# Optimization experiments

Hardware: AMD Instinct MI355X
Metric: run time of the kernel (lower is better)

## Reference

```python
import jax, jax.numpy as jnp
import numpy as np

C = 256          # channel dim, forced by self.cal (256x256)
POOL_K = 16      # feature_hw // proto_grid = 256 // 16
THRESH = 0.5
A_COEF = 0.2     # self.a


def build_cal():
    # tridiagonal 'cal' parameter from get_wight()
    cal = np.eye(C, dtype=np.float32)
    for i in range(C - 2):
        cal[i + 1, i] = 0.3
        cal[i + 1, i + 1] = 0.8
        cal[i + 1, i + 2] = 0.3
    return jnp.asarray(cal)


def setup_inputs() -> dict:
    key = jax.random.key(0)
    k1, k2, k3, k4 = jax.random.split(key, 4)
    qry = jax.random.normal(k1, (1, 1, C, 256, 256), jnp.float32)      # [way, nb, C, H, W]
    sup_x = jax.random.normal(k2, (1, 1, 1, C, 256, 256), jnp.float32)  # [way, shot, nb, C, H, W]
    sup_y = jax.random.uniform(k3, (1, 1, 1, 256, 256), jnp.float32)    # [way, shot, nb, H, W]
    s_init_seed = jax.random.randint(k4, (1, 100, 2), 0, 256)           # unused in 'gridconv'
    return {"qry": qry, "sup_x": sup_x, "sup_y": sup_y,
            "s_init_seed": s_init_seed, "cal": build_cal()}


def avg_pool(x, k):
    b, c, h, w = x.shape
    return x.reshape(b, c, h // k, k, w // k, k).mean(axis=(3, 5))


def safe_norm(x, axis, eps=1e-4):
    n = jnp.maximum(jnp.linalg.norm(x, axis=axis, keepdims=True), eps)
    return x / n


def reference(qry, sup_x, sup_y, s_init_seed, cal):
    # squeezes from the original forward
    qry = qry[:, 0]          # [1, C, H, W]
    sup_x = sup_x[0, :, 0]   # [shot, C, H, W]
    sup_y = sup_y[0]         # [shot, 1, H, W]
    ns, c, H, W = sup_x.shape

    # avg-pool support features into grid prototypes -> X: [C, N]
    nsx = avg_pool(sup_x, POOL_K)                                  # [ns, C, Gh, Gw]
    X = nsx.reshape(ns, c, -1).transpose(0, 2, 1).reshape(-1, c).T  # [C, N]

    # channel-affinity refinement: A = 1 + a * band_mask * softmax(X X^T); w3 = A * cal
    w1 = X @ X.T                                                   # [C, C]
    soft = jax.nn.softmax(w1, axis=1)
    idx = jnp.arange(c)
    mask_w = (jnp.abs(idx[:, None] - idx[None, :]) <= 1).astype(X.dtype)  # wts_near band
    A = 1.0 + A_COEF * mask_w * soft
    Xn = (A * cal) @ X                                             # [C, N]

    # pooled support mask -> proto selection
    sup_y_g = avg_pool(sup_y, POOL_K).reshape(ns, 1, -1).transpose(1, 0, 2).reshape(-1)  # [N]
    sel = sup_y_g > THRESH

    protos = safe_norm(Xn.T, axis=1)   # [N, C]
    qry_n = safe_norm(qry, axis=1)     # [1, C, H, W]

    # 1x1 conv cosine similarity; mask unselected protos (equiv. to boolean filtering)
    dists = jnp.einsum('bchw,nc->bnhw', qry_n, protos) * 20.0
    dists = jnp.where(sel[None, :, None, None], dists, jnp.float32(-1e9))
    attn = jax.nn.softmax(dists, axis=1)
    pred_grid = jnp.sum(attn * dists, axis=1, keepdims=True)       # [1, 1, H, W]
    debug_assign = jnp.argmax(dists, axis=1).astype(jnp.float32)
    return (pred_grid, debug_assign)
```

## Files before the change

### kernel.cpp

```cpp
#include <hip/hip_runtime.h>
#include <math.h>

#define CC 256
#define HW 65536
#define SS 256

#define WS_XT    0
#define WS_BORD  0
#define WS_XN    98304
#define WS_YG    163840
#define WS_INVN  164096
#define WS_SELF  164352

typedef __attribute__((ext_vector_type(8))) short short8;
typedef __attribute__((ext_vector_type(4))) float f32x4;

__device__ inline unsigned short bf16_rne(float f) {
    unsigned int u = __float_as_uint(f);
    return (unsigned short)((u + 0x7fffu + ((u >> 16) & 1u)) >> 16);
}
__device__ inline float bf16_f(unsigned short h) {
    return __uint_as_float(((unsigned int)h) << 16);
}

__global__ void pool_kernel(const float* __restrict__ sup_x,
                            const float* __restrict__ sup_y,
                            float* __restrict__ ws) {
    int blk = blockIdx.x;
    int t   = threadIdx.x;
    const float* src = (blk < CC) ? (sup_x + (size_t)blk * HW) : sup_y;

    for (int py = 0; py < 16; ++py) {
        float acc = 0.f;
        int hbase = py * 16;
        #pragma unroll
        for (int i = 0; i < 16; ++i)
            acc += src[(hbase + i) * 256 + t];
        acc += __shfl_down(acc, 8, 16);
        acc += __shfl_down(acc, 4, 16);
        acc += __shfl_down(acc, 2, 16);
        acc += __shfl_down(acc, 1, 16);
        if ((t & 15) == 0) {
            int cell = py * 16 + (t >> 4);
            float v = acc * (1.f / 256.f);
            if (blk < CC) ws[WS_XT + cell * SS + blk] = v;
            else          ws[WS_YG + cell] = v;
        }
    }
}

__global__ void calib_kernel(const float* __restrict__ cal,
                             float* __restrict__ ws) {
    int i = blockIdx.x;
    int j = threadIdx.x;
    const float* Xt = ws + WS_XT;
    float* Xn = ws + WS_XN;

    __shared__ float xi[SS];
    __shared__ float red[256];
    __shared__ float e[CC];
    __shared__ float T[3];

    xi[j] = Xt[j * SS + i];
    __syncthreads();

    float d0 = 0.f, d1 = 0.f, d2 = 0.f, d3 = 0.f;
    #pragma unroll 4
    for (int s = 0; s < SS; s += 4) {
        d0 += xi[s + 0] * Xt[(s + 0) * SS + j];
        d1 += xi[s + 1] * Xt[(s + 1) * SS + j];
        d2 += xi[s + 2] * Xt[(s + 2) * SS + j];
        d3 += xi[s + 3] * Xt[(s + 3) * SS + j];
    }
    float dot = (d0 + d1) + (d2 + d3);

    red[j] = dot; __syncthreads();
    for (int off = 128; off > 0; off >>= 1) {
        if (j < off) red[j] = fmaxf(red[j], red[j + off]);
        __syncthreads();
    }
    float m = red[0];
    __syncthreads();

    float ev = expf(dot - m);
    e[j] = ev;
    red[j] = ev; __syncthreads();
    for (int off = 128; off > 0; off >>= 1) {
        if (j < off) red[j] += red[j + off];
        __syncthreads();
    }
    float esum = red[0];
    __syncthreads();

    if (j < 3) {
        int jj = i + j - 1;
        float tv = 0.f;
        if (jj >= 0 && jj < CC) {
            float soft = e[jj] / esum;
            tv = (1.f + 0.2f * soft) * cal[i * CC + jj];
        }
        T[j] = tv;
    }
    __syncthreads();

    float v = T[1] * xi[j];
    if (i > 0)      v += T[0] * Xt[j * SS + i - 1];
    if (i < CC - 1) v += T[2] * Xt[j * SS + i + 1];
    Xn[i * SS + j] = v;
}

__global__ void prep_kernel(float* __restrict__ ws) {
    int b = blockIdx.x;
    int t = threadIdx.x;
    int nn = t & 31, cg = t >> 5;
    int n = b * 32 + nn;
    const float* Xn = ws + WS_XN;
    float s = 0.f;
    #pragma unroll 8
    for (int c = cg * 32; c < cg * 32 + 32; ++c) {
        float v = Xn[c * SS + n];
        s += v * v;
    }
    __shared__ float red[256];
    red[t] = s;
    __syncthreads();
    if (t < 32) {
        float acc = 0.f;
        #pragma unroll
        for (int g = 0; g < 8; ++g) acc += red[g * 32 + t];
        ws[WS_INVN + n] = 1.f / fmaxf(sqrtf(acc), 1e-4f);
        ws[WS_SELF + n] = (ws[WS_YG + n] > 0.5f) ? 1.f : 0.f;
    }
}

__global__ void bprep_kernel(float* __restrict__ ws) {
    int rem = (blockIdx.x & 3) * 256 + threadIdx.x;
    int c = blockIdx.x >> 2;
    int t = rem >> 6, L = rem & 63;
    int quad = L >> 4, nh = L & 15;
    int n = t * 16 + nh;
    int kb = c * 32 + quad * 8;
    const float* Xn = ws + WS_XN;

    union { unsigned short u[8]; uint4 v; } hh, mm, ll;
    #pragma unroll
    for (int j = 0; j < 8; ++j) {
        float f = Xn[(kb + j) * SS + n];
        unsigned short h = bf16_rne(f);
        float f1 = f - bf16_f(h);
        unsigned short m = bf16_rne(f1);
        float f2 = f1 - bf16_f(m);
        unsigned short l = bf16_rne(f2);
        hh.u[j] = h; mm.u[j] = m; ll.u[j] = l;
    }
    unsigned short* bord = (unsigned short*)(ws + WS_BORD);
    size_t base = ((((size_t)c * 3) * 16 + t) * 64 + L) * 8;
    *reinterpret_cast<uint4*>(&bord[base])         = hh.v;
    *reinterpret_cast<uint4*>(&bord[base + 8192])  = mm.v;
    *reinterpret_cast<uint4*>(&bord[base + 16384]) = ll.v;
}

#define NCH 8

__global__ __launch_bounds__(256)
void main_kernel(const float* __restrict__ qry,
                 const float* __restrict__ ws,
                 float* __restrict__ out) {
    __shared__ float pm[64 * 65];
    __shared__ float pa[64 * 65];
    __shared__ float invqs[64];
    __shared__ float mfin[64];
    __shared__ float afin[64];

    int tid = threadIdx.x;
    int lane = tid & 63, w = tid >> 6;
    int quad = lane >> 4, nh = lane & 15;
    int p0 = blockIdx.x * 64;
    const unsigned short* bord = (const unsigned short*)(ws + WS_BORD);

    f32x4 acc[4][4];
    #pragma unroll
    for (int mt = 0; mt < 4; ++mt)
        #pragma unroll
        for (int nt = 0; nt < 4; ++nt)
            acc[mt][nt] = (f32x4){0.f, 0.f, 0.f, 0.f};

    float qsq[4] = {0.f, 0.f, 0.f, 0.f};

    #pragma unroll 1
    for (int c = 0; c < NCH; ++c) {
        int k0 = c * 32 + quad * 8;
        short8 afr[4][3];
        #pragma unroll
        for (int mt = 0; mt < 4; ++mt) {
            float v[8];
            #pragma unroll
            for (int j = 0; j < 8; ++j)
                v[j] = qry[(size_t)(k0 + j) * HW + p0 + mt * 16 + nh];
            short8 ah, am, al;
            #pragma unroll
            for (int j = 0; j < 8; ++j) {
                qsq[mt] += v[j] * v[j];
                unsigned short h = bf16_rne(v[j]);
                float f1 = v[j] - bf16_f(h);
                unsigned short m = bf16_rne(f1);
                float f2 = f1 - bf16_f(m);
                unsigned short l = bf16_rne(f2);
                ah[j] = (short)h; am[j] = (short)m; al[j] = (short)l;
            }
            afr[mt][0] = ah; afr[mt][1] = am; afr[mt][2] = al;
        }

        const unsigned short* bc = bord + (size_t)c * 24576;
        #pragma unroll
        for (int nt = 0; nt < 4; ++nt) {
            int tg = w * 4 + nt;
            short8 bh = *(const short8*)&bc[(size_t)((0 * 16 + tg) * 64 + lane) * 8];
            short8 bm = *(const short8*)&bc[(size_t)((1 * 16 + tg) * 64 + lane) * 8];
            short8 bl = *(const short8*)&bc[(size_t)((2 * 16 + tg) * 64 + lane) * 8];
            #pragma unroll
            for (int mt = 0; mt < 4; ++mt) {
                f32x4 a = acc[mt][nt];
                a = __builtin_amdgcn_mfma_f32_16x16x32_bf16(afr[mt][2], bh, a, 0, 0, 0);
                a = __builtin_amdgcn_mfma_f32_16x16x32_bf16(afr[mt][0], bl, a, 0, 0, 0);
                a = __builtin_amdgcn_mfma_f32_16x16x32_bf16(afr[mt][1], bm, a, 0, 0, 0);
                a = __builtin_amdgcn_mfma_f32_16x16x32_bf16(afr[mt][1], bh, a, 0, 0, 0);
                a = __builtin_amdgcn_mfma_f32_16x16x32_bf16(afr[mt][0], bm, a, 0, 0, 0);
                a = __builtin_amdgcn_mfma_f32_16x16x32_bf16(afr[mt][0], bh, a, 0, 0, 0);
                acc[mt][nt] = a;
            }
        }
    }

    #pragma unroll
    for (int mt = 0; mt < 4; ++mt) {
        qsq[mt] += __shfl_xor(qsq[mt], 16);
        qsq[mt] += __shfl_xor(qsq[mt], 32);
    }
    if (w == 0 && quad == 0) {
        #pragma unroll
        for (int mt = 0; mt < 4; ++mt)
            invqs[mt * 16 + nh] = 1.f / fmaxf(sqrtf(qsq[mt]), 1e-4f);
    }

    float invn4[4], self4[4];
    #pragma unroll
    for (int nt = 0; nt < 4; ++nt) {
        int n = w * 64 + nt * 16 + nh;
        invn4[nt] = ws[WS_INVN + n];
        self4[nt] = ws[WS_SELF + n];
    }
    __syncthreads();

    #pragma unroll
    for (int mt = 0; mt < 4; ++mt) {
        #pragma unroll
        for (int r = 0; r < 4; ++r) {
            int p = mt * 16 + quad * 4 + r;
            float iq = invqs[p] * 20.f;
            float bv = -3.4e38f, ba = 1e9f;
            #pragma unroll
            for (int nt = 0; nt < 4; ++nt) {
                float d = acc[mt][nt][r] * invn4[nt] * iq;
                d = (self4[nt] > 0.5f) ? d : -1e9f;
                acc[mt][nt][r] = d;
                float na = (float)(w * 64 + nt * 16 + nh);
                if (d > bv || (d == bv && na < ba)) { bv = d; ba = na; }
            }
            pm[p * 65 + w * 16 + nh] = bv;
            pa[p * 65 + w * 16 + nh] = ba;
        }
    }
    __syncthreads();

    {
        int p = tid >> 2, q4 = tid & 3;
        float bv = -3.4e38f, ba = 1e9f;
        #pragma unroll
        for (int jj = 0; jj < 16; ++jj) {
            int cx = q4 * 16 + jj;
            float v2 = pm[p * 65 + cx];
            float a2 = pa[p * 65 + cx];
            if (v2 > bv || (v2 == bv && a2 < ba)) { bv = v2; ba = a2; }
        }
        #pragma unroll
        for (int off = 1; off < 4; off <<= 1) {
            float ov = __shfl_xor(bv, off, 4);
            float oa = __shfl_xor(ba, off, 4);
            if (ov > bv || (ov == bv && oa < ba)) { bv = ov; ba = oa; }
        }
        if (q4 == 0) { mfin[p] = bv; afin[p] = ba; }
    }
    __syncthreads();

    #pragma unroll
    for (int mt = 0; mt < 4; ++mt) {
        #pragma unroll
        for (int r = 0; r < 4; ++r) {
            int p = mt * 16 + quad * 4 + r;
            float m = mfin[p];
            float s1 = 0.f, s2 = 0.f;
            #pragma unroll
            for (int nt = 0; nt < 4; ++nt) {
                float d = acc[mt][nt][r];
                float ev = expf(d - m);
                s1 += ev;
                s2 += ev * d;
            }
            pm[p * 65 + w * 16 + nh] = s1;
            pa[p * 65 + w * 16 + nh] = s2;
        }
    }
    __syncthreads();

    {
        int p = tid >> 2, q4 = tid & 3;
        float s1 = 0.f, s2 = 0.f;
        #pragma unroll
        for (int jj = 0; jj < 16; ++jj) {
            int cx = q4 * 16 + jj;
            s1 += pm[p * 65 + cx];
            s2 += pa[p * 65 + cx];
        }
        #pragma unroll
        for (int off = 1; off < 4; off <<= 1) {
            s1 += __shfl_xor(s1, off, 4);
            s2 += __shfl_xor(s2, off, 4);
        }
        if (q4 == 0) {
            out[p0 + p]      = s2 / s1;
            out[HW + p0 + p] = afin[p];
        }
    }
}

extern "C" void kernel_launch(void* const* d_in, const int* in_sizes, int n_in,
                              void* d_out, int out_size, void* d_ws, size_t ws_size,
                              hipStream_t stream) {
    const float* qry   = (const float*)d_in[0];
    const float* sup_x = (const float*)d_in[1];
    const float* sup_y = (const float*)d_in[2];
    const float* cal   = (const float*)d_in[4];
    float* out = (float*)d_out;
    float* ws  = (float*)d_ws;

    pool_kernel<<<257, 256, 0, stream>>>(sup_x, sup_y, ws);
    calib_kernel<<<256, 256, 0, stream>>>(cal, ws);
    prep_kernel<<<8, 256, 0, stream>>>(ws);
    bprep_kernel<<<32, 256, 0, stream>>>(ws);
    main_kernel<<<HW / 64, 256, 0, stream>>>(qry, ws, out);
}
```

Measured before the change: 232.4 us.

## Prefetch query chunks, truncate bf16 splits, merge prep kernels, split pooling blocks

In the main kernel, the next channel chunk of query values is loaded into registers while the current chunk is converted and fed to MFMA, which hides global-load latency. The three-way bf16 split of the query now truncates instead of rounding to nearest, which costs fewer ALU ops per element. The prep and bprep kernels are merged into one launch, and pooling uses twice as many blocks, each covering half the rows. These changes add register pressure in the main kernel and slightly change the precision of the split.

```diff
diff --git a/kernel.cpp b/kernel.cpp
--- a/kernel.cpp
+++ b/kernel.cpp
@@ -28,9 +28,12 @@
                             float* __restrict__ ws) {
     int blk = blockIdx.x;
     int t   = threadIdx.x;
-    const float* src = (blk < CC) ? (sup_x + (size_t)blk * HW) : sup_y;
-
-    for (int py = 0; py < 16; ++py) {
+    int ch   = (blk < 512) ? (blk >> 1) : CC;
+    int pyb  = (blk < 512) ? ((blk & 1) * 8) : 0;
+    int pye  = (blk < 512) ? (pyb + 8) : 16;
+    const float* src = (blk < 512) ? (sup_x + (size_t)ch * HW) : sup_y;
+
+    for (int py = pyb; py < pye; ++py) {
         float acc = 0.f;
         int hbase = py * 16;
         #pragma unroll
@@ -43,8 +46,8 @@
         if ((t & 15) == 0) {
             int cell = py * 16 + (t >> 4);
             float v = acc * (1.f / 256.f);
-            if (blk < CC) ws[WS_XT + cell * SS + blk] = v;
-            else          ws[WS_YG + cell] = v;
+            if (blk < 512) ws[WS_XT + cell * SS + ch] = v;
+            else           ws[WS_YG + cell] = v;
         }
     }
 }
@@ -109,55 +112,55 @@
     Xn[i * SS + j] = v;
 }
 
-__global__ void prep_kernel(float* __restrict__ ws) {
-    int b = blockIdx.x;
-    int t = threadIdx.x;
-    int nn = t & 31, cg = t >> 5;
-    int n = b * 32 + nn;
+__global__ void prep_bprep_kernel(float* __restrict__ ws) {
     const float* Xn = ws + WS_XN;
-    float s = 0.f;
-    #pragma unroll 8
-    for (int c = cg * 32; c < cg * 32 + 32; ++c) {
-        float v = Xn[c * SS + n];
-        s += v * v;
-    }
-    __shared__ float red[256];
-    red[t] = s;
-    __syncthreads();
-    if (t < 32) {
-        float acc = 0.f;
-        #pragma unroll
-        for (int g = 0; g < 8; ++g) acc += red[g * 32 + t];
-        ws[WS_INVN + n] = 1.f / fmaxf(sqrtf(acc), 1e-4f);
-        ws[WS_SELF + n] = (ws[WS_YG + n] > 0.5f) ? 1.f : 0.f;
-    }
-}
-
-__global__ void bprep_kernel(float* __restrict__ ws) {
-    int rem = (blockIdx.x & 3) * 256 + threadIdx.x;
-    int c = blockIdx.x >> 2;
-    int t = rem >> 6, L = rem & 63;
-    int quad = L >> 4, nh = L & 15;
-    int n = t * 16 + nh;
-    int kb = c * 32 + quad * 8;
-    const float* Xn = ws + WS_XN;
-
-    union { unsigned short u[8]; uint4 v; } hh, mm, ll;
-    #pragma unroll
-    for (int j = 0; j < 8; ++j) {
-        float f = Xn[(kb + j) * SS + n];
-        unsigned short h = bf16_rne(f);
-        float f1 = f - bf16_f(h);
-        unsigned short m = bf16_rne(f1);
-        float f2 = f1 - bf16_f(m);
-        unsigned short l = bf16_rne(f2);
-        hh.u[j] = h; mm.u[j] = m; ll.u[j] = l;
-    }
-    unsigned short* bord = (unsigned short*)(ws + WS_BORD);
-    size_t base = ((((size_t)c * 3) * 16 + t) * 64 + L) * 8;
-    *reinterpret_cast<uint4*>(&bord[base])         = hh.v;
-    *reinterpret_cast<uint4*>(&bord[base + 8192])  = mm.v;
-    *reinterpret_cast<uint4*>(&bord[base + 16384]) = ll.v;
+    if (blockIdx.x < 8) {
+        int b = blockIdx.x;
+        int t = threadIdx.x;
+        int nn = t & 31, cg = t >> 5;
+        int n = b * 32 + nn;
+        float s = 0.f;
+        #pragma unroll 8
+        for (int c = cg * 32; c < cg * 32 + 32; ++c) {
+            float v = Xn[c * SS + n];
+            s += v * v;
+        }
+        __shared__ float red[256];
+        red[t] = s;
+        __syncthreads();
+        if (t < 32) {
+            float acc = 0.f;
+            #pragma unroll
+            for (int g = 0; g < 8; ++g) acc += red[g * 32 + t];
+            ws[WS_INVN + n] = 1.f / fmaxf(sqrtf(acc), 1e-4f);
+            ws[WS_SELF + n] = (ws[WS_YG + n] > 0.5f) ? 1.f : 0.f;
+        }
+    } else {
+        int blk = blockIdx.x - 8;
+        int rem = (blk & 3) * 256 + threadIdx.x;
+        int c = blk >> 2;
+        int t = rem >> 6, L = rem & 63;
+        int quad = L >> 4, nh = L & 15;
+        int n = t * 16 + nh;
+        int kb = c * 32 + quad * 8;
+
+        union { unsigned short u[8]; uint4 v; } hh, mm, ll;
+        #pragma unroll
+        for (int j = 0; j < 8; ++j) {
+            float f = Xn[(kb + j) * SS + n];
+            unsigned short h = bf16_rne(f);
+            float f1 = f - bf16_f(h);
+            unsigned short m = bf16_rne(f1);
+            float f2 = f1 - bf16_f(m);
+            unsigned short l = bf16_rne(f2);
+            hh.u[j] = h; mm.u[j] = m; ll.u[j] = l;
+        }
+        unsigned short* bord = (unsigned short*)(ws + WS_BORD);
+        size_t base = ((((size_t)c * 3) * 16 + t) * 64 + L) * 8;
+        *reinterpret_cast<uint4*>(&bord[base])         = hh.v;
+        *reinterpret_cast<uint4*>(&bord[base + 8192])  = mm.v;
+        *reinterpret_cast<uint4*>(&bord[base + 16384]) = ll.v;
+    }
 }
 
 #define NCH 8
@@ -177,6 +180,7 @@
     int quad = lane >> 4, nh = lane & 15;
     int p0 = blockIdx.x * 64;
     const unsigned short* bord = (const unsigned short*)(ws + WS_BORD);
+    const float* qb = qry + p0 + nh;
 
     f32x4 acc[4][4];
     #pragma unroll
@@ -187,28 +191,41 @@
 
     float qsq[4] = {0.f, 0.f, 0.f, 0.f};
 
+    float va[4][8];
+    #pragma unroll
+    for (int mt = 0; mt < 4; ++mt)
+        #pragma unroll
+        for (int j = 0; j < 8; ++j)
+            va[mt][j] = qb[(size_t)(quad * 8 + j) * HW + mt * 16];
+
     #pragma unroll 1
     for (int c = 0; c < NCH; ++c) {
-        int k0 = c * 32 + quad * 8;
         short8 afr[4][3];
         #pragma unroll
         for (int mt = 0; mt < 4; ++mt) {
-            float v[8];
-            #pragma unroll
-            for (int j = 0; j < 8; ++j)
-                v[j] = qry[(size_t)(k0 + j) * HW + p0 + mt * 16 + nh];
             short8 ah, am, al;
             #pragma unroll
             for (int j = 0; j < 8; ++j) {
-                qsq[mt] += v[j] * v[j];
-                unsigned short h = bf16_rne(v[j]);
-                float f1 = v[j] - bf16_f(h);
-                unsigned short m = bf16_rne(f1);
-                float f2 = f1 - bf16_f(m);
-                unsigned short l = bf16_rne(f2);
-                ah[j] = (short)h; am[j] = (short)m; al[j] = (short)l;
+                float f = va[mt][j];
+                qsq[mt] += f * f;
+                unsigned int u = __float_as_uint(f);
+                ah[j] = (short)(u >> 16);
+                float f1 = f - __uint_as_float(u & 0xffff0000u);
+                unsigned int u1 = __float_as_uint(f1);
+                am[j] = (short)(u1 >> 16);
+                float f2 = f1 - __uint_as_float(u1 & 0xffff0000u);
+                al[j] = (short)(__float_as_uint(f2) >> 16);
             }
             afr[mt][0] = ah; afr[mt][1] = am; afr[mt][2] = al;
+        }
+
+        if (c + 1 < NCH) {
+            int k0n = (c + 1) * 32 + quad * 8;
+            #pragma unroll
+            for (int mt = 0; mt < 4; ++mt)
+                #pragma unroll
+                for (int j = 0; j < 8; ++j)
+                    va[mt][j] = qb[(size_t)(k0n + j) * HW + mt * 16];
         }
 
         const unsigned short* bc = bord + (size_t)c * 24576;
@@ -344,9 +361,8 @@
     float* out = (float*)d_out;
     float* ws  = (float*)d_ws;
 
-    pool_kernel<<<257, 256, 0, stream>>>(sup_x, sup_y, ws);
+    pool_kernel<<<513, 256, 0, stream>>>(sup_x, sup_y, ws);
     calib_kernel<<<256, 256, 0, stream>>>(cal, ws);
-    prep_kernel<<<8, 256, 0, stream>>>(ws);
-    bprep_kernel<<<32, 256, 0, stream>>>(ws);
+    prep_bprep_kernel<<<40, 256, 0, stream>>>(ws);
     main_kernel<<<HW / 64, 256, 0, stream>>>(qry, ws, out);
 }
```

New measurement: 215.4 us. 7.3% less time.
